# Optimization experiments

Measured on AMD Instinct MI355X. Metric: run time of the kernel, lower is better.

The kernel has to match this reference:

```python
import jax, jax.numpy as jnp
import numpy as np

B, D = 32768, 256          # batch, latent_size
L, K = 4, 2048             # n_codebooks, codebook_size
BETA = 0.25                # commitment loss weight (EMA layer uses only beta term)


def setup_inputs() -> dict:
    key = jax.random.key(0)
    kx, kc = jax.random.split(key)
    x = jax.random.normal(kx, (B, D), dtype=jnp.float32)
    # per-level codebooks (EMAVQLayer.embed, xavier-normal-ish scale)
    codebooks = jax.random.normal(kc, (L, K, D), dtype=jnp.float32) * 0.1
    return {"x": x, "codebooks": codebooks}


def reference(x, codebooks):
    """RQLayer.forward (EMA variant, eval-path math; EMA buffer updates are
    side effects and do not change forward outputs)."""
    sg = jax.lax.stop_gradient
    quantized = jnp.zeros_like(x)
    loss = jnp.zeros((), x.dtype)
    unused = jnp.zeros((), jnp.int32)
    inds = []
    for l in range(L):  # small fixed number of residual levels
        c = codebooks[l]                                   # [K, D]
        dist = (jnp.sum(x * x, axis=1, keepdims=True)
                - 2.0 * (x @ c.T)
                + jnp.sum(c * c, axis=1)[None, :])
        ind = jnp.argmin(dist, axis=1)                     # [B]
        x_q = c[ind]                                       # gather [B, D]
        counts = jnp.zeros((K,), jnp.int32).at[ind].add(1)
        unused = unused + jnp.sum(counts == 0)
        loss = loss + BETA * jnp.mean((x - sg(x_q)) ** 2)
        quant = x + sg(x_q - x)                            # straight-through
        x = x - quant                                      # residual (== sg(x - x_q))
        quantized = quantized + quant
        inds.append(ind)
    return quantized, loss / L, unused, jnp.stack(inds, axis=1)
```

## Files before the change

### kernel.cpp

```cpp
#include <hip/hip_runtime.h>

#define NT 512
#define B_ 32768
#define D_ 256
#define L_ 4
#define K_ 2048
#define BM 64
#define NBLK (B_/BM)
#define BETA_ 0.25f

#define OUT_LOSS   8388608
#define OUT_UNUSED 8388609
#define OUT_INDS   8388610


__global__ __launch_bounds__(256) void rq_prep(const float* __restrict__ cb,
                                               int* __restrict__ counts,
                                               float* __restrict__ cnorm) {
  int cw = blockIdx.x * 256 + threadIdx.x;
  if (cw >= L_ * K_) return;
  counts[cw] = 0;
  const float4* cb4 = (const float4*)cb;
  float s = 0.f;
  for (int d4 = 0; d4 < 64; ++d4) {
    float4 v = cb4[(size_t)cw * 64 + d4];
    s = __fadd_rn(s, __fmul_rn(v.x, v.x));
    s = __fadd_rn(s, __fmul_rn(v.y, v.y));
    s = __fadd_rn(s, __fmul_rn(v.z, v.z));
    s = __fadd_rn(s, __fmul_rn(v.w, v.w));
  }
  cnorm[cw] = s;
}

__device__ __forceinline__ int cstp(int c) { return ((c & 7) << 3) | (c >> 3); }

template<int CTRL>
__device__ __forceinline__ float dpp_f(float v) {
  return __int_as_float(__builtin_amdgcn_update_dpp(0, __float_as_int(v), CTRL, 0xF, 0xF, true));
}
template<int CTRL>
__device__ __forceinline__ int dpp_i(int v) {
  return __builtin_amdgcn_update_dpp(0, v, CTRL, 0xF, 0xF, true);
}
#define XOR1 0xB1
#define XOR2 0x4E
#define XOR8 0x128

__global__ __attribute__((amdgpu_flat_work_group_size(NT, NT), amdgpu_waves_per_eu(2, 2)))
void rq_main(
    const float* __restrict__ x, const float* __restrict__ cb,
    float* __restrict__ out, int* __restrict__ counts,
    const float* __restrict__ cnorm, float* __restrict__ lpart) {
  __shared__ float4 xs[64][64];
  __shared__ float4 cs[64][64];
  __shared__ float  red_v[8][64];
  __shared__ int    red_i[8][64];
  __shared__ float  xxs[64];
  __shared__ int    ind_s[64];
  __shared__ float  lred[NT];

  const int tid  = threadIdx.x;
  const int lane = tid & 63;
  const int wave = tid >> 6;
  const int dg   = (lane & 3) | ((lane >> 1) & 4);
  const int p    = ((lane >> 2) & 1) | ((lane >> 3) & 6);
  const int row0 = blockIdx.x * BM;
  const float4* x4  = (const float4*)x;
  const float4* cb4 = (const float4*)cb;

  const int sl  = cstp(lane);
  const int d4r = cstp(lane ^ wave);

  {
    float4 v[8];
    #pragma unroll
    for (int it = 0; it < 8; ++it)
      v[it] = x4[(size_t)(row0 + wave + (it << 3)) * 64 + d4r];
    #pragma unroll
    for (int it = 0; it < 8; ++it)
      xs[wave + (it << 3)][lane] = v[it];
  }

  float4 st[8];
  #pragma unroll
  for (int it = 0; it < 8; ++it)
    st[it] = cb4[(size_t)(wave * 8 + it) * 64 + sl];
  #pragma unroll
  for (int it = 0; it < 8; ++it)
    cs[wave * 8 + it][lane] = st[it];

  const float4* xsp[8];
  const float4* csp[8];
  #pragma unroll
  for (int i = 0; i < 8; ++i) xsp[i] = &xs[p * 8 + i][dg ^ i];
  #pragma unroll
  for (int j = 0; j < 8; ++j) csp[j] = &cs[wave * 8 + (j ^ dg)][dg];

  float lsum = 0.f;
  const int kb = (wave << 3) | dg;
  float4* out4 = (float4*)out;

  for (int l = 0; l < L_; ++l) {
    __syncthreads();

    if (tid < 64) {
      const int sr = tid & 7;
      float s = 0.f;
      for (int d4 = 0; d4 < 64; ++d4) {
        float4 v = xs[tid][cstp(d4) ^ sr];
        s = __fadd_rn(s, __fmul_rn(v.x, v.x));
        s = __fadd_rn(s, __fmul_rn(v.y, v.y));
        s = __fadd_rn(s, __fmul_rn(v.z, v.z));
        s = __fadd_rn(s, __fmul_rn(v.w, v.w));
      }
      xxs[tid] = s;
    }
    __syncthreads();

    float xxr[8];
    #pragma unroll
    for (int i = 0; i < 8; ++i) xxr[i] = xxs[p * 8 + i];

    float bv[8]; int bi[8];
    #pragma unroll
    for (int i = 0; i < 8; ++i) { bv[i] = 3.4e38f; bi[i] = 0; }
    const float* cnl = cnorm + l * K_;

    for (int ch = 0; ch < 32; ++ch) {
      {
        int tn = l * 32 + ch + 1; if (tn > 127) tn = 127;
        const float4* src = cb4 + (size_t)tn * 4096;
        #pragma unroll
        for (int it = 0; it < 8; ++it)
          st[it] = src[(size_t)(wave * 8 + it) * 64 + sl];
      }
      const float cn = cnl[(ch << 6) + kb];

      float acc[8][8];

      {
        float4 cv[8];
        #pragma unroll
        for (int j = 0; j < 8; ++j) cv[j] = csp[j][0];
        #pragma unroll
        for (int i = 0; i < 8; ++i) {
          float4 xv = xsp[i][0];
          #pragma unroll
          for (int j = 0; j < 8; ++j) {
            float a = __fmul_rn(xv.x, cv[j].x);
            a = fmaf(xv.y, cv[j].y, a);
            a = fmaf(xv.z, cv[j].z, a);
            a = fmaf(xv.w, cv[j].w, a);
            acc[i][j] = a;
          }
        }
      }
      #pragma unroll
      for (int d = 1; d < 8; ++d) {
        float4 cv[8];
        #pragma unroll
        for (int j = 0; j < 8; ++j) cv[j] = csp[j][d << 3];
        #pragma unroll
        for (int i = 0; i < 8; ++i) {
          float4 xv = xsp[i][d << 3];
          #pragma unroll
          for (int j = 0; j < 8; ++j) {
            float a = acc[i][j];
            a = fmaf(xv.x, cv[j].x, a);
            a = fmaf(xv.y, cv[j].y, a);
            a = fmaf(xv.z, cv[j].z, a);
            a = fmaf(xv.w, cv[j].w, a);
            acc[i][j] = a;
          }
        }
      }

      #pragma unroll
      for (int it = 0; it < 8; ++it)
        cs[wave * 8 + it][lane] = st[it];

      #pragma unroll
      for (int i = 0; i < 8; ++i) {
        acc[i][0] += dpp_f<XOR1>(acc[i][1]);
        acc[i][2] += dpp_f<XOR1>(acc[i][3]);
        acc[i][4] += dpp_f<XOR1>(acc[i][5]);
        acc[i][6] += dpp_f<XOR1>(acc[i][7]);
        acc[i][0] += dpp_f<XOR2>(acc[i][2]);
        acc[i][4] += dpp_f<XOR2>(acc[i][6]);
        acc[i][0] += dpp_f<XOR8>(acc[i][4]);
      }

      const int kidx = (ch << 6) + kb;
      #pragma unroll
      for (int i = 0; i < 8; ++i) {
        float s = __fadd_rn(__fsub_rn(xxr[i], __fmul_rn(2.0f, acc[i][0])), cn);
        if (s < bv[i]) { bv[i] = s; bi[i] = kidx; }
      }
    }

    #pragma unroll
    for (int i = 0; i < 8; ++i) {
      { float pv = dpp_f<XOR1>(bv[i]); int pi = dpp_i<XOR1>(bi[i]);
        if (pv < bv[i] || (pv == bv[i] && pi < bi[i])) { bv[i] = pv; bi[i] = pi; } }
      { float pv = dpp_f<XOR2>(bv[i]); int pi = dpp_i<XOR2>(bi[i]);
        if (pv < bv[i] || (pv == bv[i] && pi < bi[i])) { bv[i] = pv; bi[i] = pi; } }
      { float pv = dpp_f<XOR8>(bv[i]); int pi = dpp_i<XOR8>(bi[i]);
        if (pv < bv[i] || (pv == bv[i] && pi < bi[i])) { bv[i] = pv; bi[i] = pi; } }
    }
    if (dg == 0) {
      #pragma unroll
      for (int i = 0; i < 8; ++i) {
        red_v[wave][p * 8 + i] = bv[i];
        red_i[wave][p * 8 + i] = bi[i];
      }
    }
    __syncthreads();
    if (tid < 64) {
      float bv_ = red_v[0][tid]; int bi_ = red_i[0][tid];
      #pragma unroll
      for (int w = 1; w < 8; ++w) {
        float v = red_v[w][tid]; int ii = red_i[w][tid];
        if (v < bv_ || (v == bv_ && ii < bi_)) { bv_ = v; bi_ = ii; }
      }
      ind_s[tid] = bi_;
      out[(size_t)OUT_INDS + (size_t)(row0 + tid) * L_ + l] = (float)bi_;
      atomicAdd(&counts[l * K_ + bi_], 1);
    }
    __syncthreads();

    #pragma unroll
    for (int it = 0; it < 8; ++it) {
      const int r = wave + (it << 3);
      const size_t oidx = (size_t)(row0 + r) * 64 + d4r;
      float4 xv = xs[r][lane];
      float4 cv = cb4[(size_t)(l * K_ + ind_s[r]) * 64 + d4r];
      float tx = __fsub_rn(cv.x, xv.x); float qx = __fadd_rn(xv.x, tx); float nx = __fsub_rn(xv.x, qx);
      float ty = __fsub_rn(cv.y, xv.y); float qy = __fadd_rn(xv.y, ty); float ny = __fsub_rn(xv.y, qy);
      float tz = __fsub_rn(cv.z, xv.z); float qz = __fadd_rn(xv.z, tz); float nz = __fsub_rn(xv.z, qz);
      float tw = __fsub_rn(cv.w, xv.w); float qw = __fadd_rn(xv.w, tw); float nw = __fsub_rn(xv.w, qw);
      float4 prev = (l == 0) ? make_float4(0.f, 0.f, 0.f, 0.f) : out4[oidx];
      out4[oidx] = make_float4(__fadd_rn(prev.x, qx), __fadd_rn(prev.y, qy),
                               __fadd_rn(prev.z, qz), __fadd_rn(prev.w, qw));
      float ex = __fsub_rn(xv.x, cv.x);
      float ey = __fsub_rn(xv.y, cv.y);
      float ez = __fsub_rn(xv.z, cv.z);
      float ew = __fsub_rn(xv.w, cv.w);
      lsum = __fadd_rn(lsum, __fmul_rn(ex, ex));
      lsum = __fadd_rn(lsum, __fmul_rn(ey, ey));
      lsum = __fadd_rn(lsum, __fmul_rn(ez, ez));
      lsum = __fadd_rn(lsum, __fmul_rn(ew, ew));
      xs[r][lane] = make_float4(nx, ny, nz, nw);
    }
  }

  lred[tid] = lsum;
  __syncthreads();
  for (int s = NT / 2; s > 0; s >>= 1) {
    if (tid < s) lred[tid] += lred[tid + s];
    __syncthreads();
  }
  if (tid == 0) lpart[blockIdx.x] = lred[0];
}

__global__ __launch_bounds__(256) void rq_final(const int* __restrict__ counts,
                                                const float* __restrict__ lpart,
                                                float* __restrict__ out) {
  __shared__ double fs[256];
  __shared__ int    is_[256];
  int tid = threadIdx.x;
  double ls = 0.0;
  for (int i = tid; i < NBLK; i += 256) ls += (double)lpart[i];
  int uz = 0;
  for (int i = tid; i < L_ * K_; i += 256) uz += (counts[i] == 0) ? 1 : 0;
  fs[tid] = ls; is_[tid] = uz;
  __syncthreads();
  for (int s = 128; s > 0; s >>= 1) {
    if (tid < s) { fs[tid] += fs[tid + s]; is_[tid] += is_[tid + s]; }
    __syncthreads();
  }
  if (tid == 0) {
    out[OUT_LOSS]   = (float)(fs[0] * (double)BETA_ / ((double)B_ * (double)D_ * (double)L_));
    out[OUT_UNUSED] = (float)is_[0];
  }
}

extern "C" void kernel_launch(void* const* d_in, const int* in_sizes, int n_in,
                              void* d_out, int out_size, void* d_ws, size_t ws_size,
                              hipStream_t stream) {
  const float* x  = (const float*)d_in[0];
  const float* cb = (const float*)d_in[1];
  float* out = (float*)d_out;
  int*   counts = (int*)d_ws;
  float* cnorm  = (float*)((char*)d_ws + 32768);
  float* lpart  = (float*)((char*)d_ws + 65536);

  rq_prep<<<(L_ * K_ + 255) / 256, 256, 0, stream>>>(cb, counts, cnorm);
  rq_main<<<NBLK, NT, 0, stream>>>(x, cb, out, counts, cnorm, lpart);
  rq_final<<<1, 256, 0, stream>>>(counts, lpart, out);
}
```

Before: 2.263 ms.

## Replace swizzled LDS layout with padded rows and reorder FMA passes

```diff
diff --git a/kernel.cpp b/kernel.cpp
--- a/kernel.cpp
+++ b/kernel.cpp
@@ -32,8 +32,6 @@
   cnorm[cw] = s;
 }
 
-__device__ __forceinline__ int cstp(int c) { return ((c & 7) << 3) | (c >> 3); }
-
 template<int CTRL>
 __device__ __forceinline__ float dpp_f(float v) {
   return __int_as_float(__builtin_amdgcn_update_dpp(0, __float_as_int(v), CTRL, 0xF, 0xF, true));
@@ -46,12 +44,22 @@
 #define XOR2 0x4E
 #define XOR8 0x128
 
-__global__ __attribute__((amdgpu_flat_work_group_size(NT, NT), amdgpu_waves_per_eu(2, 2)))
+#define FMULI(a,b,c) __fmul_rn((a),(b))
+#define FMAI(a,b,c)  fmaf((a),(b),(c))
+#define QPASS(OP, HB, CMP) \
+  _Pragma("unroll") \
+  for (int i_ = 0; i_ < 4; ++i_) { \
+    _Pragma("unroll") \
+    for (int j_ = 0; j_ < 8; ++j_) \
+      acc[(HB) + i_][j_] = OP(xv[i_].CMP, cv[j_].CMP, acc[(HB) + i_][j_]); \
+  }
+
+__global__ __attribute__((amdgpu_flat_work_group_size(NT, NT), amdgpu_waves_per_eu(1)))
 void rq_main(
     const float* __restrict__ x, const float* __restrict__ cb,
     float* __restrict__ out, int* __restrict__ counts,
     const float* __restrict__ cnorm, float* __restrict__ lpart) {
-  __shared__ float4 xs[64][64];
+  __shared__ float4 xs[64][65];
   __shared__ float4 cs[64][64];
   __shared__ float  red_v[8][64];
   __shared__ int    red_i[8][64];
@@ -68,14 +76,11 @@
   const float4* x4  = (const float4*)x;
   const float4* cb4 = (const float4*)cb;
 
-  const int sl  = cstp(lane);
-  const int d4r = cstp(lane ^ wave);
-
   {
     float4 v[8];
     #pragma unroll
     for (int it = 0; it < 8; ++it)
-      v[it] = x4[(size_t)(row0 + wave + (it << 3)) * 64 + d4r];
+      v[it] = x4[(size_t)(row0 + wave + (it << 3)) * 64 + lane];
     #pragma unroll
     for (int it = 0; it < 8; ++it)
       xs[wave + (it << 3)][lane] = v[it];
@@ -84,15 +89,13 @@
   float4 st[8];
   #pragma unroll
   for (int it = 0; it < 8; ++it)
-    st[it] = cb4[(size_t)(wave * 8 + it) * 64 + sl];
+    st[it] = cb4[(size_t)(wave * 8 + it) * 64 + lane];
   #pragma unroll
   for (int it = 0; it < 8; ++it)
     cs[wave * 8 + it][lane] = st[it];
 
-  const float4* xsp[8];
+  const float4* xb = &xs[p][dg];
   const float4* csp[8];
-  #pragma unroll
-  for (int i = 0; i < 8; ++i) xsp[i] = &xs[p * 8 + i][dg ^ i];
   #pragma unroll
   for (int j = 0; j < 8; ++j) csp[j] = &cs[wave * 8 + (j ^ dg)][dg];
 
@@ -104,10 +107,9 @@
     __syncthreads();
 
     if (tid < 64) {
-      const int sr = tid & 7;
       float s = 0.f;
       for (int d4 = 0; d4 < 64; ++d4) {
-        float4 v = xs[tid][cstp(d4) ^ sr];
+        float4 v = xs[tid][d4];
         s = __fadd_rn(s, __fmul_rn(v.x, v.x));
         s = __fadd_rn(s, __fmul_rn(v.y, v.y));
         s = __fadd_rn(s, __fmul_rn(v.z, v.z));
@@ -119,7 +121,7 @@
 
     float xxr[8];
     #pragma unroll
-    for (int i = 0; i < 8; ++i) xxr[i] = xxs[p * 8 + i];
+    for (int i = 0; i < 8; ++i) xxr[i] = xxs[(i << 3) + p];
 
     float bv[8]; int bi[8];
     #pragma unroll
@@ -132,7 +134,7 @@
         const float4* src = cb4 + (size_t)tn * 4096;
         #pragma unroll
         for (int it = 0; it < 8; ++it)
-          st[it] = src[(size_t)(wave * 8 + it) * 64 + sl];
+          st[it] = src[(size_t)(wave * 8 + it) * 64 + lane];
       }
       const float cn = cnl[(ch << 6) + kb];
 
@@ -142,42 +144,37 @@
         float4 cv[8];
         #pragma unroll
         for (int j = 0; j < 8; ++j) cv[j] = csp[j][0];
-        #pragma unroll
-        for (int i = 0; i < 8; ++i) {
-          float4 xv = xsp[i][0];
+        {
+          float4 xv[4];
           #pragma unroll
-          for (int j = 0; j < 8; ++j) {
-            float a = __fmul_rn(xv.x, cv[j].x);
-            a = fmaf(xv.y, cv[j].y, a);
-            a = fmaf(xv.z, cv[j].z, a);
-            a = fmaf(xv.w, cv[j].w, a);
-            acc[i][j] = a;
-          }
+          for (int i = 0; i < 4; ++i) xv[i] = xb[i * 520];
+          QPASS(FMULI, 0, x) QPASS(FMAI, 0, y) QPASS(FMAI, 0, z) QPASS(FMAI, 0, w)
         }
-      }
-      #pragma unroll
-      for (int d = 1; d < 8; ++d) {
+        {
+          float4 xv[4];
+          #pragma unroll
+          for (int i = 0; i < 4; ++i) xv[i] = xb[(i + 4) * 520];
+          QPASS(FMULI, 4, x) QPASS(FMAI, 4, y) QPASS(FMAI, 4, z) QPASS(FMAI, 4, w)
+        }
+      }
+      #pragma unroll
+      for (int t = 1; t < 8; ++t) {
         float4 cv[8];
         #pragma unroll
-        for (int j = 0; j < 8; ++j) cv[j] = csp[j][d << 3];
-        #pragma unroll
-        for (int i = 0; i < 8; ++i) {
-          float4 xv = xsp[i][d << 3];
+        for (int j = 0; j < 8; ++j) cv[j] = csp[j][t * 8];
+        {
+          float4 xv[4];
           #pragma unroll
-          for (int j = 0; j < 8; ++j) {
-            float a = acc[i][j];
-            a = fmaf(xv.x, cv[j].x, a);
-            a = fmaf(xv.y, cv[j].y, a);
-            a = fmaf(xv.z, cv[j].z, a);
-            a = fmaf(xv.w, cv[j].w, a);
-            acc[i][j] = a;
-          }
+          for (int i = 0; i < 4; ++i) xv[i] = xb[i * 520 + t * 8];
+          QPASS(FMAI, 0, x) QPASS(FMAI, 0, y) QPASS(FMAI, 0, z) QPASS(FMAI, 0, w)
         }
-      }
-
-      #pragma unroll
-      for (int it = 0; it < 8; ++it)
-        cs[wave * 8 + it][lane] = st[it];
+        {
+          float4 xv[4];
+          #pragma unroll
+          for (int i = 0; i < 4; ++i) xv[i] = xb[(i + 4) * 520 + t * 8];
+          QPASS(FMAI, 4, x) QPASS(FMAI, 4, y) QPASS(FMAI, 4, z) QPASS(FMAI, 4, w)
+        }
+      }
 
       #pragma unroll
       for (int i = 0; i < 8; ++i) {
@@ -196,6 +193,10 @@
         float s = __fadd_rn(__fsub_rn(xxr[i], __fmul_rn(2.0f, acc[i][0])), cn);
         if (s < bv[i]) { bv[i] = s; bi[i] = kidx; }
       }
+
+      #pragma unroll
+      for (int it = 0; it < 8; ++it)
+        cs[wave * 8 + it][lane] = st[it];
     }
 
     #pragma unroll
@@ -210,8 +211,8 @@
     if (dg == 0) {
       #pragma unroll
       for (int i = 0; i < 8; ++i) {
-        red_v[wave][p * 8 + i] = bv[i];
-        red_i[wave][p * 8 + i] = bi[i];
+        red_v[wave][(i << 3) + p] = bv[i];
+        red_i[wave][(i << 3) + p] = bi[i];
       }
     }
     __syncthreads();
@@ -231,9 +232,9 @@
     #pragma unroll
     for (int it = 0; it < 8; ++it) {
       const int r = wave + (it << 3);
-      const size_t oidx = (size_t)(row0 + r) * 64 + d4r;
+      const size_t oidx = (size_t)(row0 + r) * 64 + lane;
       float4 xv = xs[r][lane];
-      float4 cv = cb4[(size_t)(l * K_ + ind_s[r]) * 64 + d4r];
+      float4 cv = cb4[(size_t)(l * K_ + ind_s[r]) * 64 + lane];
       float tx = __fsub_rn(cv.x, xv.x); float qx = __fadd_rn(xv.x, tx); float nx = __fsub_rn(xv.x, qx);
       float ty = __fsub_rn(cv.y, xv.y); float qy = __fadd_rn(xv.y, ty); float ny = __fsub_rn(xv.y, qy);
       float tz = __fsub_rn(cv.z, xv.z); float qz = __fadd_rn(xv.z, tz); float nz = __fsub_rn(xv.z, qz);
```

New measurement: 2.049 ms. 1.1x faster.
